# Performance work log

Hardware: AMD Instinct MI355X
Metric: run time of the kernel (lower is better)

## Reference

```python
import jax, jax.numpy as jnp
import numpy as np

N_NODES = 50000
N_EDGES = 1250000
D = 64
EPS = 1e-07


def setup_inputs() -> dict:
    key = jax.random.key(0)
    ks = jax.random.split(key, 10)
    return {
        "node_feats": jax.random.normal(ks[0], (N_NODES, D), jnp.float32),
        "emb0": jax.random.normal(ks[1], (8, D), jnp.float32),
        "emb1": jax.random.normal(ks[2], (4, D), jnp.float32),
        "W": jax.random.normal(ks[3], (D, D), jnp.float32) / np.sqrt(D),
        "b": jnp.zeros((D,), jnp.float32),
        "beta": jnp.ones((1,), jnp.float32),
        "scale": jnp.ones((1,), jnp.float32),
        "src": jax.random.randint(ks[4], (N_EDGES,), 0, N_NODES),
        "dst": jax.random.randint(ks[5], (N_EDGES,), 0, N_NODES),
        "edge_feat0": jax.random.randint(ks[6], (N_EDGES,), 0, 8),
        "edge_feat1": jax.random.randint(ks[7], (N_EDGES,), 0, 4),
    }


def reference(node_feats, emb0, emb1, W, b, beta, scale, src, dst, edge_feat0, edge_feat1):
    n = node_feats.shape[0]
    # edge embeddings summed over categorical feature types
    e = emb0[edge_feat0] + emb1[edge_feat1]              # [E, D]
    # u_add_e then relu + eps
    m = jnp.maximum(node_feats[src] + e, 0.0) + EPS      # [E, D]
    # edge softmax over edges sharing the same destination (per feature dim)
    logits = m * beta                                    # [E, D]
    mx = jax.ops.segment_max(logits, dst, num_segments=n)
    ex = jnp.exp(logits - mx[dst])
    denom = jax.ops.segment_sum(ex, dst, num_segments=n)
    a = ex / denom[dst]                                  # [E, D]
    # scatter-sum aggregation of m * a to destination nodes
    msg = jax.ops.segment_sum(m * a, dst, num_segments=n)  # [N, D]
    # MessageNorm: L2-normalize msg, rescale by ||node_feats|| * scale
    msg_unit = msg / jnp.maximum(
        jnp.linalg.norm(msg, axis=-1, keepdims=True), 1e-12)
    feats_norm = jnp.linalg.norm(node_feats, axis=-1, keepdims=True)
    msg = msg_unit * feats_norm * scale
    # residual + single-layer MLP
    feats = node_feats + msg
    return feats @ W + b
```

## Files before the change

kernel.cpp:

```cpp
#include <hip/hip_runtime.h>

#define NN 50000
#define NE 1250000
#define DD 64
#define KRF 1563
#define BSH 5
#define SCAPF 1024
#define SCSHF 10
#define CPAD 5


__global__ __launch_bounds__(512) void k_part(
    const int4* __restrict__ src4, const int4* __restrict__ dst4,
    const int4* __restrict__ ef04, const int4* __restrict__ ef14,
    const float* __restrict__ W, float* __restrict__ Wt,
    int* __restrict__ rcur, unsigned* __restrict__ staging)
{
    __shared__ int hist[KRF], rbase[KRF], cur[KRF];
    const int t  = threadIdx.x;
    const int gb = blockIdx.x;

    for (int i = t; i < KRF; i += 512) { hist[i] = 0; cur[i] = 0; }
    if (gb == 0)
        for (int i = t; i < 4096; i += 512)
            Wt[(i & 63) * DD + (i >> 6)] = W[i];
    __syncthreads();

    unsigned pay[4];
    int rr[4];
#pragma unroll
    for (int u = 0; u < 4; ++u) rr[u] = -1;

    const int i4 = gb * 512 + t;
    if (i4 < NE / 4) {
        const int4 s  = src4[i4], d = dst4[i4];
        const int4 f0 = ef04[i4], f1 = ef14[i4];
        const int ds[4] = {d.x, d.y, d.z, d.w};
        const int ss[4] = {s.x, s.y, s.z, s.w};
        const int a0[4] = {f0.x, f0.y, f0.z, f0.w};
        const int a1[4] = {f1.x, f1.y, f1.z, f1.w};
#pragma unroll
        for (int u = 0; u < 4; ++u) {
            rr[u]  = ds[u] >> BSH;
            pay[u] = (unsigned)ss[u] | ((unsigned)(a1[u] * 8 + a0[u]) << 16)
                     | ((unsigned)(ds[u] & 31) << 21);
        }
    }
#pragma unroll
    for (int u = 0; u < 4; ++u)
        if (rr[u] >= 0) atomicAdd(&hist[rr[u]], 1);
    __syncthreads();

    for (int i = t; i < KRF; i += 512) {
        const int h = hist[i];
        if (h) rbase[i] = atomicAdd(&rcur[i << CPAD], h);
    }
    __syncthreads();

#pragma unroll
    for (int u = 0; u < 4; ++u) {
        if (rr[u] >= 0) {
            const int r   = rr[u];
            const int pos = rbase[r] + atomicAdd(&cur[r], 1);
            if (pos < SCAPF) staging[(r << SCSHF) + pos] = pay[u];
        }
    }
}

__global__ __launch_bounds__(256, 4) void genconv_agg(
    const float* __restrict__ nf,
    const float* __restrict__ emb0, const float* __restrict__ emb1,
    const float* __restrict__ Wt,  const float* __restrict__ b,
    const float* __restrict__ beta_p, const float* __restrict__ scale_p,
    const unsigned* __restrict__ staging, const int* __restrict__ rcur,
    float* __restrict__ out)
{
    __shared__ float emb_s[32 * DD];
    __shared__ float feat_s[4][DD];
    __shared__ unsigned buck[32 * DD];
    __shared__ int ldeg[32];

    const int t    = threadIdx.x;
    const int w    = t >> 6;
    const int lane = t & 63;
    const int bin  = blockIdx.x;
    const int base_node = bin << BSH;

    if (t < 32) ldeg[t] = 0;
    for (int i = t; i < 32 * DD; i += 256) {
        const int rr = i >> 6, c = i & 63;
        emb_s[i] = emb0[(rr & 7) * DD + c] + emb1[(rr >> 3) * DD + c];
    }

    float4 wc[16];
#pragma unroll
    for (int k = 0; k < 16; ++k)
        wc[k] = *(const float4*)(Wt + lane * DD + 4 * k);

    const float bias  = b[lane];
    const float beta  = beta_p[0];
    const float scale = scale_p[0];
    __syncthreads();

    const int ne = min(rcur[bin << CPAD], SCAPF);
    const unsigned* sg = staging + (bin << SCSHF);
    for (int i = t; i < ne; i += 256) {
        const unsigned p = sg[i];
        const int dl  = (p >> 21) & 31;
        const int pos = atomicAdd(&ldeg[dl], 1);
        if (pos < DD) buck[(dl << 6) + pos] = p & 0x1FFFFFu;
    }
    __syncthreads();

    const int nl0 = w << 3;
    unsigned pl = buck[(nl0 << 6) + lane];
    int cn = min(ldeg[nl0], DD);
    int node = base_node + nl0;
    float f = (node < NN) ? nf[(size_t)node * DD + lane] : 0.0f;

    for (int i = 0; i < 8; ++i) {
        const int nl = nl0 + i;
        node = base_node + nl;

        unsigned pl_n = 0u;
        int cn_n = 0;
        float f_n = 0.0f;
        if (i < 7) {
            pl_n = buck[((nl + 1) << 6) + lane];
            cn_n = ldeg[nl + 1];
            if (node + 1 < NN)
                f_n = nf[(size_t)(node + 1) * DD + lane];
        }

        float num = 0.0f, den = 0.0f;
        for (int j = 0; j < cn; j += 16) {
            float a[16];
            unsigned qv[16];
#pragma unroll
            for (int u = 0; u < 16; ++u) {
                const unsigned qq =
                    (unsigned)__builtin_amdgcn_readlane((int)pl, (j + u) & 63);
                qv[u] = qq;
                const int sidx = min((int)(qq & 0xFFFFu), NN - 1);
                a[u] = nf[(size_t)sidx * DD + lane];
            }
#pragma unroll
            for (int u = 0; u < 16; ++u) {
                const float eb = emb_s[(((qv[u] >> 16) & 31) << 6) + lane];
                const float m  = fmaxf(a[u] + eb, 0.0f) + 1e-7f;
                float x = __expf(beta * m);
                x = (j + u < cn) ? x : 0.0f;
                den += x;
                num = fmaf(m, x, num);
            }
        }

        const float msg = (den > 0.0f) ? num / den : 0.0f;

        float ss = msg * msg;
        float fs = f * f;
#pragma unroll
        for (int m = 32; m >= 1; m >>= 1) {
            ss += __shfl_xor(ss, m, 64);
            fs += __shfl_xor(fs, m, 64);
        }

        const float feat =
            f + msg * (1.0f / fmaxf(sqrtf(ss), 1e-12f)) * sqrtf(fs) * scale;

        feat_s[w][lane] = feat;

        float acc = bias;
#pragma unroll
        for (int k = 0; k < 16; ++k) {
            const float4 fv = *(const float4*)&feat_s[w][4 * k];
            acc = fmaf(fv.x, wc[k].x, acc);
            acc = fmaf(fv.y, wc[k].y, acc);
            acc = fmaf(fv.z, wc[k].z, acc);
            acc = fmaf(fv.w, wc[k].w, acc);
        }
        if (node < NN)
            out[(size_t)node * DD + lane] = acc;

        pl = pl_n;
        cn = min(cn_n, DD);
        f  = f_n;
    }
}

extern "C" void kernel_launch(void* const* d_in, const int* in_sizes, int n_in,
                              void* d_out, int out_size, void* d_ws, size_t ws_size,
                              hipStream_t stream)
{
    const float* nf    = (const float*)d_in[0];
    const float* emb0  = (const float*)d_in[1];
    const float* emb1  = (const float*)d_in[2];
    const float* W     = (const float*)d_in[3];
    const float* b     = (const float*)d_in[4];
    const float* beta  = (const float*)d_in[5];
    const float* scale = (const float*)d_in[6];
    const int* src = (const int*)d_in[7];
    const int* dst = (const int*)d_in[8];
    const int* ef0 = (const int*)d_in[9];
    const int* ef1 = (const int*)d_in[10];

    int*      rcur    = (int*)d_ws;
    float*    Wt      = (float*)(rcur + (KRF << CPAD));
    unsigned* staging = (unsigned*)(Wt + 4096);

    hipMemsetAsync(rcur, 0, (size_t)(KRF << CPAD) * sizeof(int), stream);

    k_part<<<(NE / 4 + 511) / 512, 512, 0, stream>>>(
        (const int4*)src, (const int4*)dst, (const int4*)ef0, (const int4*)ef1,
        W, Wt, rcur, staging);

    genconv_agg<<<KRF, 256, 0, stream>>>(
        nf, emb0, emb1, Wt, b, beta, scale, staging, rcur, (float*)d_out);
}
```

Before: 211.8 us.

## Replace shared-memory histogram partitioning with direct global atomics per edge

The partition kernel no longer builds a per-block LDS histogram of destination bins with block-level reservation. Each edge now does its own global atomicAdd on a padded per-bin counter, which removes the three __syncthreads phases and the LDS use. Block size drops to 256 and counter padding shrinks from 32 to 16 ints. The cost is about 1.25M global atomics on only 1563 counters instead of one atomic per bin per block, so contention on those counters may rise.

```diff
diff --git a/kernel.cpp b/kernel.cpp
--- a/kernel.cpp
+++ b/kernel.cpp
@@ -7,63 +7,40 @@
 #define BSH 5
 #define SCAPF 1024
 #define SCSHF 10
-#define CPAD 5
+#define CPAD 4
 
 
-__global__ __launch_bounds__(512) void k_part(
+__global__ __launch_bounds__(256) void k_part(
     const int4* __restrict__ src4, const int4* __restrict__ dst4,
     const int4* __restrict__ ef04, const int4* __restrict__ ef14,
     const float* __restrict__ W, float* __restrict__ Wt,
     int* __restrict__ rcur, unsigned* __restrict__ staging)
 {
-    __shared__ int hist[KRF], rbase[KRF], cur[KRF];
     const int t  = threadIdx.x;
     const int gb = blockIdx.x;
 
-    for (int i = t; i < KRF; i += 512) { hist[i] = 0; cur[i] = 0; }
     if (gb == 0)
-        for (int i = t; i < 4096; i += 512)
+        for (int i = t; i < 4096; i += 256)
             Wt[(i & 63) * DD + (i >> 6)] = W[i];
-    __syncthreads();
 
-    unsigned pay[4];
-    int rr[4];
-#pragma unroll
-    for (int u = 0; u < 4; ++u) rr[u] = -1;
+    const int i4 = gb * 256 + t;
+    if (i4 >= NE / 4) return;
 
-    const int i4 = gb * 512 + t;
-    if (i4 < NE / 4) {
-        const int4 s  = src4[i4], d = dst4[i4];
-        const int4 f0 = ef04[i4], f1 = ef14[i4];
-        const int ds[4] = {d.x, d.y, d.z, d.w};
-        const int ss[4] = {s.x, s.y, s.z, s.w};
-        const int a0[4] = {f0.x, f0.y, f0.z, f0.w};
-        const int a1[4] = {f1.x, f1.y, f1.z, f1.w};
-#pragma unroll
-        for (int u = 0; u < 4; ++u) {
-            rr[u]  = ds[u] >> BSH;
-            pay[u] = (unsigned)ss[u] | ((unsigned)(a1[u] * 8 + a0[u]) << 16)
-                     | ((unsigned)(ds[u] & 31) << 21);
-        }
-    }
-#pragma unroll
-    for (int u = 0; u < 4; ++u)
-        if (rr[u] >= 0) atomicAdd(&hist[rr[u]], 1);
-    __syncthreads();
-
-    for (int i = t; i < KRF; i += 512) {
-        const int h = hist[i];
-        if (h) rbase[i] = atomicAdd(&rcur[i << CPAD], h);
-    }
-    __syncthreads();
+    const int4 s  = src4[i4], d = dst4[i4];
+    const int4 f0 = ef04[i4], f1 = ef14[i4];
+    const int ds[4] = {d.x, d.y, d.z, d.w};
+    const int ss[4] = {s.x, s.y, s.z, s.w};
+    const int a0[4] = {f0.x, f0.y, f0.z, f0.w};
+    const int a1[4] = {f1.x, f1.y, f1.z, f1.w};
 
 #pragma unroll
     for (int u = 0; u < 4; ++u) {
-        if (rr[u] >= 0) {
-            const int r   = rr[u];
-            const int pos = rbase[r] + atomicAdd(&cur[r], 1);
-            if (pos < SCAPF) staging[(r << SCSHF) + pos] = pay[u];
-        }
+        const int bin = ds[u] >> BSH;
+        const unsigned pay = (unsigned)ss[u]
+            | ((unsigned)(a1[u] * 8 + a0[u]) << 16)
+            | ((unsigned)(ds[u] & 31) << 21);
+        const int pos = atomicAdd(&rcur[bin << CPAD], 1);
+        if (pos < SCAPF) staging[(bin << SCSHF) + pos] = pay;
     }
 }
 
@@ -210,7 +187,7 @@
 
     hipMemsetAsync(rcur, 0, (size_t)(KRF << CPAD) * sizeof(int), stream);
 
-    k_part<<<(NE / 4 + 511) / 512, 512, 0, stream>>>(
+    k_part<<<(NE / 4 + 255) / 256, 256, 0, stream>>>(
         (const int4*)src, (const int4*)dst, (const int4*)ef0, (const int4*)ef1,
         W, Wt, rcur, staging);
 
```

Result: slower. 237.8 us (+12.2%).
